# Performance work log

Hardware: AMD Instinct MI355X
Metric: run time of the kernel (lower is better)

## Reference

```python
import jax, jax.numpy as jnp
import numpy as np

TEMPERATURE = 0.04
LAMBDA_KOLEO = 0.1
EPS_NORM = 1e-12
EPS_KOLEO = 1e-9


def setup_inputs() -> dict:
    key = jax.random.key(0)
    k1, k2 = jax.random.split(key)
    N, D = 8192, 512
    z1 = jax.random.normal(k1, (N, D), dtype=jnp.float32)
    z2 = jax.random.normal(k2, (N, D), dtype=jnp.float32)
    return {"z1": z1, "z2": z2}


def _l2_normalize(x):
    # matches F.normalize(x, dim=1) with default eps=1e-12
    n = jnp.linalg.norm(x, axis=1, keepdims=True)
    return x / jnp.maximum(n, EPS_NORM)


def _infonce(queries, keys, temperature):
    # [N, N] similarity logits; labels are the diagonal
    logits = (queries @ keys.T) / temperature
    logp = jax.nn.log_softmax(logits, axis=1)
    return -jnp.mean(jnp.diagonal(logp))


def _koleo(emb):
    # pairwise euclidean distances via gram trick (matches torch.cdist p=2)
    sq = jnp.sum(emb * emb, axis=1)
    d2 = sq[:, None] + sq[None, :] - 2.0 * (emb @ emb.T)
    d = jnp.sqrt(jnp.maximum(d2, 0.0))
    N = emb.shape[0]
    eye = jnp.eye(N, dtype=bool)
    d = jnp.where(eye, jnp.inf, d)
    min_d = jnp.min(d, axis=1)
    return -jnp.mean(jnp.log(min_d + EPS_KOLEO))


def reference(z1, z2):
    z1 = _l2_normalize(z1)
    z2 = _l2_normalize(z2)
    loss_12 = _infonce(z1, z2, TEMPERATURE)
    loss_21 = _infonce(z2, z1, TEMPERATURE)
    loss_contrastive = (loss_12 + loss_21) / 2
    koleo_1 = _koleo(z1)
    koleo_2 = _koleo(z2)
    loss_koleo = (koleo_1 + koleo_2) / 2
    total_loss = loss_contrastive + LAMBDA_KOLEO * loss_koleo
    return total_loss
```

## Files before the change

### kernel.cpp

```cpp
#include <hip/hip_runtime.h>
#include <hip/hip_bf16.h>
#include <hip/hip_fp8.h>
#include <math.h>

#define N 8192
#define D 512
#define BM 128
#define BK 64
#define NSTRIP 64
#define S_BLOCKS (NSTRIP * NSTRIP)
#define TRI (NSTRIP * (NSTRIP + 1) / 2)
#define G_BLOCKS (2 * TRI)
#define SG_BLOCKS (S_BLOCKS + G_BLOCKS)

typedef float f32x4 __attribute__((ext_vector_type(4)));
typedef long l2 __attribute__((ext_vector_type(2)));

__device__ inline void gload_lds16(const void* g, void* l) {
  __builtin_amdgcn_global_load_lds(
      (const __attribute__((address_space(1))) void*)g,
      (__attribute__((address_space(3))) void*)l, 16, 0, 0);
}

__global__ __launch_bounds__(256) void norm_kernel(
    const float* __restrict__ z1, const float* __restrict__ z2,
    unsigned char* __restrict__ q1, unsigned char* __restrict__ q2,
    float* __restrict__ diag, float* __restrict__ out) {
  int row = blockIdx.x;
  int t = threadIdx.x;
  if (row == 0 && t == 0) out[0] = 0.0f;
  const float* a = z1 + (size_t)row * D;
  const float* b = z2 + (size_t)row * D;
  float va[2], vb[2];
  float ss1 = 0.f, ss2 = 0.f, dd = 0.f;
#pragma unroll
  for (int i = 0; i < 2; i++) {
    float x = a[t + 256 * i];
    float y = b[t + 256 * i];
    va[i] = x; vb[i] = y;
    ss1 += x * x; ss2 += y * y; dd += x * y;
  }
#pragma unroll
  for (int off = 1; off < 64; off <<= 1) {
    ss1 += __shfl_xor(ss1, off);
    ss2 += __shfl_xor(ss2, off);
    dd  += __shfl_xor(dd,  off);
  }
  __shared__ float red[3][4];
  int wv = t >> 6;
  if ((t & 63) == 0) { red[0][wv] = ss1; red[1][wv] = ss2; red[2][wv] = dd; }
  __syncthreads();
  ss1 = red[0][0] + red[0][1] + red[0][2] + red[0][3];
  ss2 = red[1][0] + red[1][1] + red[1][2] + red[1][3];
  dd  = red[2][0] + red[2][1] + red[2][2] + red[2][3];
  float i1 = 1.0f / fmaxf(sqrtf(ss1), 1e-12f);
  float i2 = 1.0f / fmaxf(sqrtf(ss2), 1e-12f);
#pragma unroll
  for (int i = 0; i < 2; i++) {
    __hip_fp8_e4m3 c1((float)(va[i] * i1));
    __hip_fp8_e4m3 c2((float)(vb[i] * i2));
    q1[(size_t)row * D + t + 256 * i] = c1.__x;
    q2[(size_t)row * D + t + 256 * i] = c2.__x;
  }
  if (t == 0) diag[row] = dd * i1 * i2;
}

__device__ __forceinline__ void stage_tile(
    const unsigned char* __restrict__ P, int base, int k0,
    unsigned char* T, int t) {
#pragma unroll
  for (int it = 0; it < 2; it++) {
    int s = it * 256 + t;
    int row = s >> 2, cs = s & 3;
    int src = cs ^ ((row >> 1) & 3);
    gload_lds16(P + (size_t)(base + row) * D + k0 + src * 16, &T[s * 16]);
  }
}

__device__ __forceinline__ void mm_tile_fp8(
    const unsigned char* __restrict__ X, const unsigned char* __restrict__ Y,
    int r0, int c0, unsigned char* At0, unsigned char* Bt0,
    unsigned char* At1, unsigned char* Bt1, f32x4 (&acc)[4][4],
    int t, int lr, int quad, int rw, int cw) {
  const f32x4 vzero = {0.0f, 0.0f, 0.0f, 0.0f};
#pragma unroll
  for (int i = 0; i < 4; i++)
#pragma unroll
    for (int j = 0; j < 4; j++) acc[i][j] = vzero;

  stage_tile(X, r0, 0, At0, t);
  stage_tile(Y, c0, 0, Bt0, t);

  for (int kc = 0; kc < 8; kc++) {
    unsigned char* Ac = (kc & 1) ? At1 : At0;
    unsigned char* Bc = (kc & 1) ? Bt1 : Bt0;
    unsigned char* An = (kc & 1) ? At0 : At1;
    unsigned char* Bn = (kc & 1) ? Bt0 : Bt1;
    __syncthreads();
    if (kc < 7) {
      stage_tile(X, r0, (kc + 1) * BK, An, t);
      stage_tile(Y, c0, (kc + 1) * BK, Bn, t);
    }
    l2 af[4], bf[4];
#pragma unroll
    for (int i = 0; i < 4; i++) {
      int row = rw * 64 + i * 16 + lr;
      int ps = quad ^ ((row >> 1) & 3);
      af[i] = *(const l2*)&Ac[row * 64 + ps * 16];
    }
#pragma unroll
    for (int j = 0; j < 4; j++) {
      int row = cw * 64 + j * 16 + lr;
      int ps = quad ^ ((row >> 1) & 3);
      bf[j] = *(const l2*)&Bc[row * 64 + ps * 16];
    }
#pragma unroll
    for (int i = 0; i < 4; i++)
#pragma unroll
      for (int j = 0; j < 4; j++)
        acc[i][j] = __builtin_amdgcn_mfma_f32_16x16x32_fp8_fp8(af[i].x, bf[j].x, acc[i][j], 0, 0, 0);
#pragma unroll
    for (int i = 0; i < 4; i++)
#pragma unroll
      for (int j = 0; j < 4; j++)
        acc[i][j] = __builtin_amdgcn_mfma_f32_16x16x32_fp8_fp8(af[i].y, bf[j].y, acc[i][j], 0, 0, 0);
  }
}

__global__ __launch_bounds__(256, 3) void sg_kernel(
    const unsigned char* __restrict__ q1, const unsigned char* __restrict__ q2,
    float* __restrict__ rowS, float* __restrict__ colS,
    float* __restrict__ partG) {
  __shared__ unsigned char At0[BM * BK];
  __shared__ unsigned char Bt0[BM * BK];
  __shared__ unsigned char At1[BM * BK];
  __shared__ unsigned char Bt1[BM * BK];
  __shared__ float redA[2][BM];
  __shared__ float redB[2][BM];

  int bx = blockIdx.x;
  int t = threadIdx.x;
  int lane = t & 63;
  int wave = t >> 6;
  int quad = lane >> 4;
  int lr = lane & 15;
  int rw = wave >> 1;
  int cw = wave & 1;
  const float scale = 1.4426950408889634f / 0.04f;

  bool smode = bx < S_BLOCKS;
  const unsigned char* X;
  const unsigned char* Y;
  int r0, c0, ga = 0, gb = 0, gg = 0;
  bool diagb = false;
  if (smode) {
    r0 = (bx >> 6) * BM;
    c0 = (bx & 63) * BM;
    X = q1; Y = q2;
  } else {
    int gx = bx - S_BLOCKS;
    gg = (gx >= TRI) ? 1 : 0;
    int tri = gx - gg * TRI;
    int a = (int)((sqrtf(8.0f * (float)tri + 1.0f) - 1.0f) * 0.5f);
    while ((a + 1) * (a + 2) / 2 <= tri) a++;
    while (a * (a + 1) / 2 > tri) a--;
    int b = tri - a * (a + 1) / 2;
    ga = a; gb = b;
    X = gg ? q2 : q1; Y = X;
    r0 = a * BM;
    c0 = b * BM;
    diagb = (a == b);
  }

  f32x4 acc[4][4];
  mm_tile_fp8(X, Y, r0, c0, At0, Bt0, At1, Bt1, acc, t, lr, quad, rw, cw);

  if (smode) {
    float rowacc[4][4];
    float colacc[4] = {0.0f, 0.0f, 0.0f, 0.0f};
#pragma unroll
    for (int i = 0; i < 4; i++)
#pragma unroll
      for (int r = 0; r < 4; r++) rowacc[i][r] = 0.0f;
#pragma unroll
    for (int i = 0; i < 4; i++)
#pragma unroll
      for (int j = 0; j < 4; j++)
#pragma unroll
        for (int r = 0; r < 4; r++) {
          float e = __builtin_amdgcn_exp2f(acc[i][j][r] * scale);
          rowacc[i][r] += e;
          colacc[j] += e;
        }
#pragma unroll
    for (int j = 0; j < 4; j++) {
      colacc[j] += __shfl_xor(colacc[j], 16);
      colacc[j] += __shfl_xor(colacc[j], 32);
    }
    __syncthreads();
    if (lane < 16) {
#pragma unroll
      for (int j = 0; j < 4; j++) redA[rw][cw * 64 + j * 16 + lr] = colacc[j];
    }
    __syncthreads();
    if (t < BM) colS[(size_t)(r0 >> 7) * N + c0 + t] = redA[0][t] + redA[1][t];

#pragma unroll
    for (int i = 0; i < 4; i++)
#pragma unroll
      for (int r = 0; r < 4; r++) {
        float v = rowacc[i][r];
#pragma unroll
        for (int off = 1; off < 16; off <<= 1) v += __shfl_xor(v, off);
        if (lr == 0) redB[cw][rw * 64 + i * 16 + quad * 4 + r] = v;
      }
    __syncthreads();
    if (t < BM) rowS[(size_t)(c0 >> 7) * N + r0 + t] = redB[0][t] + redB[1][t];
  } else {
    __syncthreads();
#pragma unroll
    for (int i = 0; i < 4; i++)
#pragma unroll
      for (int r = 0; r < 4; r++) {
        int rr = rw * 64 + i * 16 + quad * 4 + r;
        float v = -3.0e38f;
#pragma unroll
        for (int j = 0; j < 4; j++) {
          float x = acc[i][j][r];
          int cc = cw * 64 + j * 16 + lr;
          if (diagb && cc == rr) x = -3.0e38f;
          v = fmaxf(v, x);
        }
#pragma unroll
        for (int off = 1; off < 16; off <<= 1) v = fmaxf(v, __shfl_xor(v, off));
        if (lr == 0) redA[cw][rr] = v;
      }
    __syncthreads();
    if (t < BM)
      partG[((size_t)(gg * NSTRIP + gb)) * N + r0 + t] = fmaxf(redA[0][t], redA[1][t]);

    if (!diagb) {
#pragma unroll
      for (int j = 0; j < 4; j++) {
        float m = acc[0][j][0];
#pragma unroll
        for (int i = 0; i < 4; i++)
#pragma unroll
          for (int r = 0; r < 4; r++) m = fmaxf(m, acc[i][j][r]);
        m = fmaxf(m, __shfl_xor(m, 16));
        m = fmaxf(m, __shfl_xor(m, 32));
        if (lane < 16) redB[rw][cw * 64 + j * 16 + lr] = m;
      }
      __syncthreads();
      if (t < BM)
        partG[((size_t)(gg * NSTRIP + ga)) * N + c0 + t] = fmaxf(redB[0][t], redB[1][t]);
    }
  }
}

__global__ __launch_bounds__(256) void combine_kernel(
    const float* __restrict__ diag,
    const float* __restrict__ rowS, const float* __restrict__ colS,
    const float* __restrict__ partG, float* __restrict__ out) {
  const float invT = 25.0f;
  int i = blockIdx.x * 256 + threadIdx.x;

  float s = 0.0f;
  for (int q = 0; q < NSTRIP; q++) s += rowS[(size_t)q * N + i];
  float a12 = logf(s) - diag[i] * invT;

  s = 0.0f;
  for (int o = 0; o < NSTRIP; o++) s += colS[(size_t)o * N + i];
  float a21 = logf(s) - diag[i] * invT;

  float g1 = -3.0e38f, g2 = -3.0e38f;
  for (int o = 0; o < NSTRIP; o++) {
    g1 = fmaxf(g1, partG[(size_t)o * N + i]);
    g2 = fmaxf(g2, partG[(size_t)(NSTRIP + o) * N + i]);
  }
  float k1 = logf(sqrtf(fmaxf(2.0f - 2.0f * g1, 0.0f)) + 1e-9f);
  float k2 = logf(sqrtf(fmaxf(2.0f - 2.0f * g2, 0.0f)) + 1e-9f);

  float c = 0.5f * (a12 + a21) / (float)N - 0.1f * 0.5f * (k1 + k2) / (float)N;
#pragma unroll
  for (int off = 1; off < 64; off <<= 1) c += __shfl_xor(c, off);
  __shared__ float fr[4];
  int wv = threadIdx.x >> 6;
  if ((threadIdx.x & 63) == 0) fr[wv] = c;
  __syncthreads();
  if (threadIdx.x == 0)
    atomicAdd(out, fr[0] + fr[1] + fr[2] + fr[3]);
}

extern "C" void kernel_launch(void* const* d_in, const int* in_sizes, int n_in,
                              void* d_out, int out_size, void* d_ws, size_t ws_size,
                              hipStream_t stream) {
  const float* z1 = (const float*)d_in[0];
  const float* z2 = (const float*)d_in[1];
  char* w = (char*)d_ws;
  unsigned char* q1 = (unsigned char*)w; w += (size_t)N * D;
  unsigned char* q2 = (unsigned char*)w; w += (size_t)N * D;
  float* diag = (float*)w;   w += (size_t)N * sizeof(float);
  float* rowS = (float*)w;   w += (size_t)NSTRIP * N * sizeof(float);
  float* colS = (float*)w;   w += (size_t)NSTRIP * N * sizeof(float);
  float* partG = (float*)w;  w += (size_t)2 * NSTRIP * N * sizeof(float);
  float* out = (float*)d_out;

  norm_kernel<<<N, 256, 0, stream>>>(z1, z2, q1, q2, diag, out);
  sg_kernel<<<SG_BLOCKS, 256, 0, stream>>>(q1, q2, rowS, colS, partG);
  combine_kernel<<<N / 256, 256, 0, stream>>>(diag, rowS, colS, partG, out);
}
```

Before: 187.2 us.

## Switch FP8 GEMM to 32x32x64 scaled MFMA with XCD-aware block remap

Result: slower. 216.4 us (+15.6%).

```diff
diff --git a/kernel.cpp b/kernel.cpp
--- a/kernel.cpp
+++ b/kernel.cpp
@@ -13,8 +13,9 @@
 #define G_BLOCKS (2 * TRI)
 #define SG_BLOCKS (S_BLOCKS + G_BLOCKS)
 
-typedef float f32x4 __attribute__((ext_vector_type(4)));
-typedef long l2 __attribute__((ext_vector_type(2)));
+typedef float f32x16 __attribute__((ext_vector_type(16)));
+typedef int i32x4 __attribute__((ext_vector_type(4)));
+typedef int i32x8 __attribute__((ext_vector_type(8)));
 
 __device__ inline void gload_lds16(const void* g, void* l) {
   __builtin_amdgcn_global_load_lds(
@@ -77,20 +78,38 @@
   }
 }
 
-__device__ __forceinline__ void mm_tile_fp8(
+__device__ __forceinline__ void mm_tile_mx(
     const unsigned char* __restrict__ X, const unsigned char* __restrict__ Y,
     int r0, int c0, unsigned char* At0, unsigned char* Bt0,
-    unsigned char* At1, unsigned char* Bt1, f32x4 (&acc)[4][4],
-    int t, int lr, int quad, int rw, int cw) {
-  const f32x4 vzero = {0.0f, 0.0f, 0.0f, 0.0f};
-#pragma unroll
-  for (int i = 0; i < 4; i++)
-#pragma unroll
-    for (int j = 0; j < 4; j++) acc[i][j] = vzero;
+    unsigned char* At1, unsigned char* Bt1, f32x16 (&acc)[2][2],
+    int t, int l31, int kl, int rw, int cw) {
+#pragma unroll
+  for (int i = 0; i < 2; i++)
+#pragma unroll
+    for (int j = 0; j < 2; j++)
+#pragma unroll
+      for (int r = 0; r < 16; r++) acc[i][j][r] = 0.0f;
+
+  int offA[2][2], offB[2][2];
+#pragma unroll
+  for (int i = 0; i < 2; i++) {
+    int row = rw * 64 + i * 32 + l31;
+    int sw = (row >> 1) & 3;
+    offA[i][0] = row * 64 + (((kl << 1) | 0) ^ sw) * 16;
+    offA[i][1] = row * 64 + (((kl << 1) | 1) ^ sw) * 16;
+  }
+#pragma unroll
+  for (int j = 0; j < 2; j++) {
+    int row = cw * 64 + j * 32 + l31;
+    int sw = (row >> 1) & 3;
+    offB[j][0] = row * 64 + (((kl << 1) | 0) ^ sw) * 16;
+    offB[j][1] = row * 64 + (((kl << 1) | 1) ^ sw) * 16;
+  }
 
   stage_tile(X, r0, 0, At0, t);
   stage_tile(Y, c0, 0, Bt0, t);
 
+#pragma unroll 2
   for (int kc = 0; kc < 8; kc++) {
     unsigned char* Ac = (kc & 1) ? At1 : At0;
     unsigned char* Bc = (kc & 1) ? Bt1 : Bt0;
@@ -101,29 +120,26 @@
       stage_tile(X, r0, (kc + 1) * BK, An, t);
       stage_tile(Y, c0, (kc + 1) * BK, Bn, t);
     }
-    l2 af[4], bf[4];
-#pragma unroll
-    for (int i = 0; i < 4; i++) {
-      int row = rw * 64 + i * 16 + lr;
-      int ps = quad ^ ((row >> 1) & 3);
-      af[i] = *(const l2*)&Ac[row * 64 + ps * 16];
-    }
-#pragma unroll
-    for (int j = 0; j < 4; j++) {
-      int row = cw * 64 + j * 16 + lr;
-      int ps = quad ^ ((row >> 1) & 3);
-      bf[j] = *(const l2*)&Bc[row * 64 + ps * 16];
-    }
-#pragma unroll
-    for (int i = 0; i < 4; i++)
-#pragma unroll
-      for (int j = 0; j < 4; j++)
-        acc[i][j] = __builtin_amdgcn_mfma_f32_16x16x32_fp8_fp8(af[i].x, bf[j].x, acc[i][j], 0, 0, 0);
-#pragma unroll
-    for (int i = 0; i < 4; i++)
-#pragma unroll
-      for (int j = 0; j < 4; j++)
-        acc[i][j] = __builtin_amdgcn_mfma_f32_16x16x32_fp8_fp8(af[i].y, bf[j].y, acc[i][j], 0, 0, 0);
+    i32x8 af[2], bf[2];
+#pragma unroll
+    for (int i = 0; i < 2; i++) {
+      i32x4 lo = *(const i32x4*)&Ac[offA[i][0]];
+      i32x4 hi = *(const i32x4*)&Ac[offA[i][1]];
+      af[i] = __builtin_shufflevector(lo, hi, 0, 1, 2, 3, 4, 5, 6, 7);
+    }
+#pragma unroll
+    for (int j = 0; j < 2; j++) {
+      i32x4 lo = *(const i32x4*)&Bc[offB[j][0]];
+      i32x4 hi = *(const i32x4*)&Bc[offB[j][1]];
+      bf[j] = __builtin_shufflevector(lo, hi, 0, 1, 2, 3, 4, 5, 6, 7);
+    }
+#pragma unroll
+    for (int i = 0; i < 2; i++)
+#pragma unroll
+      for (int j = 0; j < 2; j++)
+        acc[i][j] = __builtin_amdgcn_mfma_scale_f32_32x32x64_f8f6f4(
+            af[i], bf[j], acc[i][j], 0 , 0 ,
+            0, 0x7F7F7F7F, 0, 0x7F7F7F7F);
   }
 }
 
@@ -138,12 +154,14 @@
   __shared__ float redA[2][BM];
   __shared__ float redB[2][BM];
 
-  int bx = blockIdx.x;
+  int bxr = blockIdx.x;
+  int bx = (bxr & 7) * (SG_BLOCKS / 8) + (bxr >> 3);
+
   int t = threadIdx.x;
   int lane = t & 63;
   int wave = t >> 6;
-  int quad = lane >> 4;
-  int lr = lane & 15;
+  int l31 = lane & 31;
+  int h = lane >> 5;
   int rw = wave >> 1;
   int cw = wave & 1;
   const float scale = 1.4426950408889634f / 0.04f;
@@ -172,87 +190,94 @@
     diagb = (a == b);
   }
 
-  f32x4 acc[4][4];
-  mm_tile_fp8(X, Y, r0, c0, At0, Bt0, At1, Bt1, acc, t, lr, quad, rw, cw);
+  f32x16 acc[2][2];
+  mm_tile_mx(X, Y, r0, c0, At0, Bt0, At1, Bt1, acc, t, l31, h, rw, cw);
 
   if (smode) {
-    float rowacc[4][4];
-    float colacc[4] = {0.0f, 0.0f, 0.0f, 0.0f};
-#pragma unroll
-    for (int i = 0; i < 4; i++)
-#pragma unroll
-      for (int r = 0; r < 4; r++) rowacc[i][r] = 0.0f;
-#pragma unroll
-    for (int i = 0; i < 4; i++)
-#pragma unroll
-      for (int j = 0; j < 4; j++)
-#pragma unroll
-        for (int r = 0; r < 4; r++) {
-          float e = __builtin_amdgcn_exp2f(acc[i][j][r] * scale);
-          rowacc[i][r] += e;
-          colacc[j] += e;
+    float csum[2] = {0.0f, 0.0f};
+#pragma unroll
+    for (int i = 0; i < 2; i++) {
+      float rsum[16];
+#pragma unroll
+      for (int reg = 0; reg < 16; reg++) rsum[reg] = 0.0f;
+#pragma unroll
+      for (int j = 0; j < 2; j++)
+#pragma unroll
+        for (int reg = 0; reg < 16; reg++) {
+          float e = __builtin_amdgcn_exp2f(acc[i][j][reg] * scale);
+          rsum[reg] += e;
+          csum[j] += e;
         }
 #pragma unroll
-    for (int j = 0; j < 4; j++) {
-      colacc[j] += __shfl_xor(colacc[j], 16);
-      colacc[j] += __shfl_xor(colacc[j], 32);
+      for (int reg = 0; reg < 16; reg++) {
+#pragma unroll
+        for (int off = 1; off < 32; off <<= 1) rsum[reg] += __shfl_xor(rsum[reg], off);
+      }
+      if (l31 == 0) {
+#pragma unroll
+        for (int reg = 0; reg < 16; reg++) {
+          int rloc = (reg & 3) + 8 * (reg >> 2) + 4 * h;
+          redB[cw][rw * 64 + i * 32 + rloc] = rsum[reg];
+        }
+      }
+    }
+#pragma unroll
+    for (int j = 0; j < 2; j++) {
+      csum[j] += __shfl_xor(csum[j], 32);
+      if (h == 0) redA[rw][cw * 64 + j * 32 + l31] = csum[j];
     }
     __syncthreads();
-    if (lane < 16) {
-#pragma unroll
-      for (int j = 0; j < 4; j++) redA[rw][cw * 64 + j * 16 + lr] = colacc[j];
-    }
-    __syncthreads();
-    if (t < BM) colS[(size_t)(r0 >> 7) * N + c0 + t] = redA[0][t] + redA[1][t];
-
-#pragma unroll
-    for (int i = 0; i < 4; i++)
-#pragma unroll
-      for (int r = 0; r < 4; r++) {
-        float v = rowacc[i][r];
-#pragma unroll
-        for (int off = 1; off < 16; off <<= 1) v += __shfl_xor(v, off);
-        if (lr == 0) redB[cw][rw * 64 + i * 16 + quad * 4 + r] = v;
-      }
-    __syncthreads();
-    if (t < BM) rowS[(size_t)(c0 >> 7) * N + r0 + t] = redB[0][t] + redB[1][t];
+    if (t < BM) {
+      colS[(size_t)(r0 >> 7) * N + c0 + t] = redA[0][t] + redA[1][t];
+      rowS[(size_t)(c0 >> 7) * N + r0 + t] = redB[0][t] + redB[1][t];
+    }
   } else {
-    __syncthreads();
-#pragma unroll
-    for (int i = 0; i < 4; i++)
-#pragma unroll
-      for (int r = 0; r < 4; r++) {
-        int rr = rw * 64 + i * 16 + quad * 4 + r;
+#pragma unroll
+    for (int i = 0; i < 2; i++) {
+      float rmax[16];
+#pragma unroll
+      for (int reg = 0; reg < 16; reg++) {
+        int rloc = (reg & 3) + 8 * (reg >> 2) + 4 * h;
+        int rr = rw * 64 + i * 32 + rloc;
         float v = -3.0e38f;
 #pragma unroll
-        for (int j = 0; j < 4; j++) {
-          float x = acc[i][j][r];
-          int cc = cw * 64 + j * 16 + lr;
+        for (int j = 0; j < 2; j++) {
+          float x = acc[i][j][reg];
+          int cc = cw * 64 + j * 32 + l31;
           if (diagb && cc == rr) x = -3.0e38f;
           v = fmaxf(v, x);
         }
-#pragma unroll
-        for (int off = 1; off < 16; off <<= 1) v = fmaxf(v, __shfl_xor(v, off));
-        if (lr == 0) redA[cw][rr] = v;
-      }
+        rmax[reg] = v;
+      }
+#pragma unroll
+      for (int reg = 0; reg < 16; reg++) {
+#pragma unroll
+        for (int off = 1; off < 32; off <<= 1) rmax[reg] = fmaxf(rmax[reg], __shfl_xor(rmax[reg], off));
+      }
+      if (l31 == 0) {
+#pragma unroll
+        for (int reg = 0; reg < 16; reg++) {
+          int rloc = (reg & 3) + 8 * (reg >> 2) + 4 * h;
+          redA[cw][rw * 64 + i * 32 + rloc] = rmax[reg];
+        }
+      }
+    }
+    if (!diagb) {
+#pragma unroll
+      for (int j = 0; j < 2; j++) {
+        float m = -3.0e38f;
+#pragma unroll
+        for (int i = 0; i < 2; i++)
+#pragma unroll
+          for (int reg = 0; reg < 16; reg++) m = fmaxf(m, acc[i][j][reg]);
+        m = fmaxf(m, __shfl_xor(m, 32));
+        if (h == 0) redB[rw][cw * 64 + j * 32 + l31] = m;
+      }
+    }
     __syncthreads();
-    if (t < BM)
+    if (t < BM) {
       partG[((size_t)(gg * NSTRIP + gb)) * N + r0 + t] = fmaxf(redA[0][t], redA[1][t]);
-
-    if (!diagb) {
-#pragma unroll
-      for (int j = 0; j < 4; j++) {
-        float m = acc[0][j][0];
-#pragma unroll
-        for (int i = 0; i < 4; i++)
-#pragma unroll
-          for (int r = 0; r < 4; r++) m = fmaxf(m, acc[i][j][r]);
-        m = fmaxf(m, __shfl_xor(m, 16));
-        m = fmaxf(m, __shfl_xor(m, 32));
-        if (lane < 16) redB[rw][cw * 64 + j * 16 + lr] = m;
-      }
-      __syncthreads();
-      if (t < BM)
+      if (!diagb)
         partG[((size_t)(gg * NSTRIP + ga)) * N + c0 + t] = fmaxf(redB[0][t], redB[1][t]);
     }
   }
```
